# Optimization experiments

Hardware: AMD Instinct MI355X
Metric: run time of the kernel (lower is better)

Reference implementation:

```python
import jax, jax.numpy as jnp
import numpy as np

DIM_IN, DIM_Q, DIM_K, DIM_S, DIM_MLP_S, L, B = 512, 128, 128, 256, 128, 512, 32


def setup_inputs() -> dict:
    key = jax.random.key(0)
    ks = jax.random.split(key, 16)
    s = lambda fan_in: 1.0 / np.sqrt(fan_in)
    inp = {
        "query": jax.random.normal(ks[0], (B, L, DIM_IN), jnp.float32),
        "key": jax.random.normal(ks[1], (B, L, DIM_IN), jnp.float32),
        "value": jax.random.normal(ks[2], (B, L, DIM_IN), jnp.float32),
        "sf": jax.random.normal(ks[3], (B, DIM_S), jnp.float32),
        "atten_mask": jax.random.randint(ks[4], (B, L, L), 0, 2).astype(bool),
        # linear weights stored (in, out); y = x @ W + b
        "Wq": jax.random.normal(ks[5], (DIM_IN, DIM_Q), jnp.float32) * s(DIM_IN),
        "bq": jnp.zeros((DIM_Q,), jnp.float32),
        "Wk": jax.random.normal(ks[6], (DIM_IN, DIM_K), jnp.float32) * s(DIM_IN),
        "bk": jnp.zeros((DIM_K,), jnp.float32),
        "Wv": jax.random.normal(ks[7], (DIM_IN, DIM_K), jnp.float32) * s(DIM_IN),
        "bv": jnp.zeros((DIM_K,), jnp.float32),
        "Wb1": jax.random.normal(ks[8], (DIM_S, DIM_MLP_S), jnp.float32) * s(DIM_S),
        "bb1": jnp.zeros((DIM_MLP_S,), jnp.float32),
        "Wb2": jax.random.normal(ks[9], (DIM_MLP_S, L * L), jnp.float32) * s(DIM_MLP_S),
        "bb2": jnp.zeros((L * L,), jnp.float32),
    }
    return inp


def reference(query, key, value, sf, atten_mask, Wq, bq, Wk, bk, Wv, bv, Wb1, bb1, Wb2, bb2):
    b, l, d = query.shape
    q = query @ Wq + bq          # [b, l, dim_q]
    k = key @ Wk + bk            # [b, l, dim_k]
    v = value @ Wv + bv          # [b, l, dim_k]
    # bias MLP: Linear -> ReLU -> Linear, reshaped to [b, l, l]
    bias = (jax.nn.relu(sf @ Wb1 + bb1) @ Wb2 + bb2).reshape(b, l, l)
    scale = q.shape[-1] ** 0.5
    scores = jnp.einsum("bld,bmd->blm", q, k) / scale
    # faithful to masked_fill_(mask, 1e-9): masked positions become 1e-9, NOT -inf
    scores = jnp.where(atten_mask, jnp.asarray(1e-9, scores.dtype), scores)
    attn = jax.nn.softmax(scores, axis=-1) + bias   # bias added AFTER softmax
    out = jnp.einsum("blm,bmd->bld", attn, v)
    return out
```

## Files before the change

kernel.cpp:

```cpp
#include <hip/hip_runtime.h>


typedef unsigned int   u32;
typedef unsigned short u16;
typedef __attribute__((ext_vector_type(8))) short bf16x8;
typedef __attribute__((ext_vector_type(4))) float f32x4;
typedef __attribute__((ext_vector_type(4))) u32   u32x4;

__device__ __forceinline__ float B2F(u16 x) { return __uint_as_float(((u32)x) << 16); }
__device__ __forceinline__ u16 f2bf(float f) {
    u32 u = __float_as_uint(f);
    return (u16)((u + 0x7fffu + ((u >> 16) & 1u)) >> 16);
}

__global__ __launch_bounds__(256) void prep(
    const void* __restrict__ mask, u32* __restrict__ flag, int detN,
    const float* __restrict__ Wq, const float* __restrict__ Wk, const float* __restrict__ Wv,
    u16* __restrict__ WT,
    const float* __restrict__ sf, const float* __restrict__ Wb1,
    const float* __restrict__ bb1, float* __restrict__ hT)
{
    __shared__ u16 Ts[64][136];
    const int blk = blockIdx.x, tid = threadIdx.x;

    if (blk < detN) {
        const u32* m = (const u32*)mask;
        u32 any = 0;
#pragma unroll
        for (int it = 0; it < 16; ++it) {
            const size_t t = ((size_t)blk * 16 + it) * 256 + tid;
#pragma unroll
            for (int l = 0; l < 4; ++l) any |= (m[t * 4 + l] > 1u) ? 1u : 0u;
        }
        if (__ballot(any)) {
            if ((tid & 63) == 0) atomicOr(flag, 1u);
        }
        return;
    }
    if (blk < detN + 24) {
        const int widx = blk - detN;
        const int s = widx >> 3, kt = widx & 7;
        const float* W = (s == 0) ? Wq : (s == 1) ? Wk : Wv;
        {
            const int kk = tid >> 2, nseg = tid & 3;
            const float4* src = (const float4*)(W + (size_t)(kt * 64 + kk) * 128 + nseg * 32);
#pragma unroll
            for (int j = 0; j < 8; ++j) {
                float4 v = src[j];
                Ts[kk][nseg * 32 + j * 4 + 0] = f2bf(v.x);
                Ts[kk][nseg * 32 + j * 4 + 1] = f2bf(v.y);
                Ts[kk][nseg * 32 + j * 4 + 2] = f2bf(v.z);
                Ts[kk][nseg * 32 + j * 4 + 3] = f2bf(v.w);
            }
        }
        __syncthreads();
        {
            const int n = tid >> 1, kseg = tid & 1;
            u32 pk[16];
#pragma unroll
            for (int j = 0; j < 16; ++j)
                pk[j] = (u32)Ts[kseg * 32 + 2 * j][n] | ((u32)Ts[kseg * 32 + 2 * j + 1][n] << 16);
            u32x4* dst = (u32x4*)(WT + (size_t)s * 65536 + (size_t)n * 512 + kt * 64 + kseg * 32);
            dst[0] = (u32x4){pk[0], pk[1], pk[2], pk[3]};
            dst[1] = (u32x4){pk[4], pk[5], pk[6], pk[7]};
            dst[2] = (u32x4){pk[8], pk[9], pk[10], pk[11]};
            dst[3] = (u32x4){pk[12], pk[13], pk[14], pk[15]};
        }
        return;
    }
    {
        const int t = (blk - detN - 24) * 256 + tid;
        const int b = t >> 7, n = t & 127;
        float acc = bb1[n];
        for (int m = 0; m < 256; ++m)
            acc += sf[b * 256 + m] * Wb1[m * 128 + n];
        hT[n * 32 + b] = fmaxf(acc, 0.0f);
    }
}

__global__ __launch_bounds__(256) void mid(
    const float* __restrict__ Xq, const float* __restrict__ Xk, const float* __restrict__ Xv,
    const u16* __restrict__ WT,
    const float* __restrict__ Bq, const float* __restrict__ Bk, const float* __restrict__ Bv,
    u16* __restrict__ Yq, u16* __restrict__ Yk, u16* __restrict__ YvT,
    const float* __restrict__ hT, const float* __restrict__ Wb2,
    const float* __restrict__ bb2, u16* __restrict__ biasb,
    const void* __restrict__ mask, const u32* __restrict__ flag, int mode,
    int docanon, unsigned char* __restrict__ canonbuf)
{
    __shared__ u16 Xs[64][72];
    const int blk = blockIdx.x, tid = threadIdx.x;

    if (blk < 1024) {
        const size_t n = (size_t)blk * 256 + tid;
        float acc[32];
        {
            const float bb = bb2[n];
#pragma unroll
            for (int b = 0; b < 32; ++b) acc[b] = bb;
        }
#pragma unroll 16
        for (int m = 0; m < 128; ++m) {
            const float wv = Wb2[(size_t)m * 262144 + n];
            const float* hrow = hT + m * 32;
#pragma unroll
            for (int b = 0; b < 32; ++b) acc[b] += wv * hrow[b];
        }
#pragma unroll
        for (int b = 0; b < 32; ++b)
            biasb[(size_t)b * 262144 + n] = f2bf(acc[b]);
        return;
    }

    if (blk < 1792) {
        const int pidx = blk - 1024;
        const int s = pidx >> 8;
        const int R0 = (pidx & 255) * 64;
        const float* X; const float* Bi;
        if (s == 0)      { X = Xq; Bi = Bq; }
        else if (s == 1) { X = Xk; Bi = Bk; }
        else             { X = Xv; Bi = Bv; }
        const u16* Wn = WT + (size_t)s * 65536;

        const int w    = tid >> 6;
        const int lane = tid & 63;
        const int c    = lane & 15;
        const int qd   = lane >> 4;

        f32x4 acc[8];
#pragma unroll
        for (int t = 0; t < 8; ++t) acc[t] = (f32x4){0.f, 0.f, 0.f, 0.f};

        for (int kc = 0; kc < 8; ++kc) {
            __syncthreads();
            {
                const int row = tid >> 2, seg = tid & 3;
                const float4* src = (const float4*)(X + (size_t)(R0 + row) * 512 + kc * 64 + seg * 16);
                float4 v0 = src[0], v1 = src[1], v2 = src[2], v3 = src[3];
                u32 pk[8];
                pk[0] = (u32)f2bf(v0.x) | ((u32)f2bf(v0.y) << 16);
                pk[1] = (u32)f2bf(v0.z) | ((u32)f2bf(v0.w) << 16);
                pk[2] = (u32)f2bf(v1.x) | ((u32)f2bf(v1.y) << 16);
                pk[3] = (u32)f2bf(v1.z) | ((u32)f2bf(v1.w) << 16);
                pk[4] = (u32)f2bf(v2.x) | ((u32)f2bf(v2.y) << 16);
                pk[5] = (u32)f2bf(v2.z) | ((u32)f2bf(v2.w) << 16);
                pk[6] = (u32)f2bf(v3.x) | ((u32)f2bf(v3.y) << 16);
                pk[7] = (u32)f2bf(v3.z) | ((u32)f2bf(v3.w) << 16);
                u32x4* dst = (u32x4*)&Xs[row][seg * 16];
                dst[0] = (u32x4){pk[0], pk[1], pk[2], pk[3]};
                dst[1] = (u32x4){pk[4], pk[5], pk[6], pk[7]};
            }
            __syncthreads();

#pragma unroll
            for (int ks = 0; ks < 2; ++ks) {
                if (s < 2) {
                    const bf16x8 a = *(const bf16x8*)&Xs[w * 16 + c][ks * 32 + qd * 8];
#pragma unroll
                    for (int nt = 0; nt < 8; ++nt) {
                        const bf16x8 b = *(const bf16x8*)(Wn + (size_t)(nt * 16 + c) * 512
                                                          + kc * 64 + ks * 32 + qd * 8);
                        acc[nt] = __builtin_amdgcn_mfma_f32_16x16x32_bf16(a, b, acc[nt], 0, 0, 0);
                    }
                } else {
#pragma unroll
                    for (int t = 0; t < 2; ++t) {
                        const bf16x8 a = *(const bf16x8*)(Wn + (size_t)((2 * w + t) * 16 + c) * 512
                                                          + kc * 64 + ks * 32 + qd * 8);
#pragma unroll
                        for (int it = 0; it < 4; ++it) {
                            const bf16x8 b = *(const bf16x8*)&Xs[it * 16 + c][ks * 32 + qd * 8];
                            acc[t * 4 + it] = __builtin_amdgcn_mfma_f32_16x16x32_bf16(a, b, acc[t * 4 + it], 0, 0, 0);
                        }
                    }
                }
            }
        }

        if (s < 2) {
            u16* Y = (s == 0) ? Yq : Yk;
#pragma unroll
            for (int nt = 0; nt < 8; ++nt) {
                const float bn = Bi[nt * 16 + c];
#pragma unroll
                for (int r = 0; r < 4; ++r)
                    Y[(size_t)(R0 + w * 16 + qd * 4 + r) * 128 + nt * 16 + c] = f2bf(acc[nt][r] + bn);
            }
        } else {
            const int bb = (pidx & 255) >> 3, il0 = R0 & 511;
#pragma unroll
            for (int t = 0; t < 2; ++t)
#pragma unroll
                for (int r = 0; r < 4; ++r) {
                    const int d = (2 * w + t) * 16 + qd * 4 + r;
                    const float bd = Bi[d];
#pragma unroll
                    for (int it = 0; it < 4; ++it)
                        YvT[(size_t)bb * 65536 + (size_t)d * 512 + il0 + it * 16 + c] =
                            f2bf(acc[t * 4 + it][r] + bd);
                }
        }
        return;
    }

    if (docanon) {
        const int cb = blk - 1792;
        const bool i32src = (mode == 2) || (mode == 0 && *flag == 0);
#pragma unroll
        for (int it = 0; it < 8; ++it) {
            const size_t base = ((size_t)cb * 8 + it) * 4096 + (size_t)tid * 16;
            u32 wq[4];
            if (i32src) {
                const int* mi = (const int*)mask + base;
#pragma unroll
                for (int q = 0; q < 4; ++q) {
                    const int4 v = *(const int4*)(mi + q * 4);
                    wq[q] = (v.x ? 1u : 0u) | ((v.y ? 1u : 0u) << 8)
                          | ((v.z ? 1u : 0u) << 16) | ((v.w ? 1u : 0u) << 24);
                }
            } else {
                const u32x4 v = *(const u32x4*)((const unsigned char*)mask + base);
#pragma unroll
                for (int q = 0; q < 4; ++q) {
                    const u32 x = v[q];
                    wq[q] = (((x & 0x7F7F7F7Fu) + 0x7F7F7F7Fu) | x) >> 7 & 0x01010101u;
                }
            }
            *(u32x4*)(canonbuf + base) = (u32x4){wq[0], wq[1], wq[2], wq[3]};
        }
    }
}

__global__ __launch_bounds__(512, 2) void attn_mfma8(
    const u16* __restrict__ qb, const u16* __restrict__ kb, const u16* __restrict__ vTb,
    const unsigned char* __restrict__ canon, const u16* __restrict__ biasb,
    float* __restrict__ out)
{
    __shared__ alignas(16) u16 Ks[2][64 * 136];
    __shared__ alignas(16) u16 Ps[2][64 * 72];
    __shared__ alignas(16) u16 Vs[2][128 * 72];
    __shared__ alignas(16) u16 Bs[2][64 * 72];
    __shared__ float redm[2][64];
    __shared__ float reds[2][64];

    const int tid  = threadIdx.x;
    const int g    = tid >> 8;
    const int gtid = tid & 255;
    const int wl   = (tid >> 6) & 3;
    const int lane = tid & 63;
    const int c    = lane & 15;
    const int qd   = lane >> 4;
    const int bb   = blockIdx.x & 31;
    const int it   = blockIdx.x >> 5;
    const int i0   = it * 64;

    bf16x8 qf[4];
    {
        const u16* qp = qb + ((size_t)bb * 512 + i0 + wl * 16 + c) * 128 + qd * 8;
#pragma unroll
        for (int kc = 0; kc < 4; ++kc) qf[kc] = *(const bf16x8*)(qp + kc * 32);
    }

    const int kr_ = gtid >> 2, ksg = gtid & 3;
    const u16* kbase = kb + ((size_t)bb * 512 + g * 256) * 128;
    {
        const u32x4* src = (const u32x4*)(kbase + (size_t)kr_ * 128 + ksg * 32);
        u32x4 k0 = src[0], k1 = src[1], k2 = src[2], k3 = src[3];
        u32x4* dst = (u32x4*)&Ks[g][kr_ * 136 + ksg * 32];
        dst[0] = k0; dst[1] = k1; dst[2] = k2; dst[3] = k3;
    }
    __syncthreads();

    f32x4 S[4][4];
#pragma unroll
    for (int jt = 0; jt < 4; ++jt)
#pragma unroll
        for (int jj = 0; jj < 4; ++jj) S[jt][jj] = (f32x4){0.f, 0.f, 0.f, 0.f};

#pragma unroll
    for (int jt = 0; jt < 4; ++jt) {
        u32x4 k0, k1, k2, k3;
        if (jt < 3) {
            const u32x4* src = (const u32x4*)(kbase + ((size_t)(jt + 1) * 64 + kr_) * 128 + ksg * 32);
            k0 = src[0]; k1 = src[1]; k2 = src[2]; k3 = src[3];
        }
#pragma unroll
        for (int kc = 0; kc < 4; ++kc) {
            const bf16x8 a = qf[kc];
#pragma unroll
            for (int jj = 0; jj < 4; ++jj) {
                const bf16x8 b = *(const bf16x8*)&Ks[g][(jj * 16 + c) * 136 + kc * 32 + qd * 8];
                S[jt][jj] = __builtin_amdgcn_mfma_f32_16x16x32_bf16(a, b, S[jt][jj], 0, 0, 0);
            }
        }
        if (jt < 3) {
            __syncthreads();
            u32x4* dst = (u32x4*)&Ks[g][kr_ * 136 + ksg * 32];
            dst[0] = k0; dst[1] = k1; dst[2] = k2; dst[3] = k3;
            __syncthreads();
        }
    }

    const int vd = gtid >> 1, vsg = gtid & 1;
    const int brw = gtid >> 2, bsg = gtid & 3;
    const u16* vbase = vTb + (size_t)bb * 65536;
    const u16* bbase = biasb + (size_t)bb * 262144;
    u32x4 vr0, vr1, vr2, vr3, br0, br1;
    {
        const u32x4* sv = (const u32x4*)(vbase + (size_t)vd * 512 + (g * 4) * 64 + vsg * 32);
        vr0 = sv[0]; vr1 = sv[1]; vr2 = sv[2]; vr3 = sv[3];
        const u32x4* sb = (const u32x4*)(bbase + (size_t)(i0 + brw) * 512 + (g * 4) * 64 + bsg * 16);
        br0 = sb[0]; br1 = sb[1];
    }

    const float sc = 0.08838834764831845f;
    float lm[4];
#pragma unroll
    for (int r = 0; r < 4; ++r) {
        const int lrow = wl * 16 + qd * 4 + r;
        const unsigned char* cp = canon + ((size_t)bb * 512 + i0 + lrow) * 512 + g * 256;
        float mx = -3.4e38f;
#pragma unroll
        for (int jt = 0; jt < 4; ++jt)
#pragma unroll
            for (int jj = 0; jj < 4; ++jj) {
                float s = S[jt][jj][r] * sc;
                if (cp[jt * 64 + jj * 16 + c]) s = 1e-9f;
                S[jt][jj][r] = s;
                mx = fmaxf(mx, s);
            }
#pragma unroll
        for (int o = 1; o < 16; o <<= 1) mx = fmaxf(mx, __shfl_xor(mx, o, 64));
        lm[r] = mx;
    }
    if (c == 0) {
#pragma unroll
        for (int r = 0; r < 4; ++r) redm[g][wl * 16 + qd * 4 + r] = lm[r];
    }
    __syncthreads();
    float ls[4];
#pragma unroll
    for (int r = 0; r < 4; ++r) {
        const int lrow = wl * 16 + qd * 4 + r;
        const float gmx = fmaxf(redm[0][lrow], redm[1][lrow]);
        float sm = 0.f;
#pragma unroll
        for (int jt = 0; jt < 4; ++jt)
#pragma unroll
            for (int jj = 0; jj < 4; ++jj) {
                const float e = __expf(S[jt][jj][r] - gmx);
                S[jt][jj][r] = e;
                sm += e;
            }
#pragma unroll
        for (int o = 1; o < 16; o <<= 1) sm += __shfl_xor(sm, o, 64);
        ls[r] = sm;
    }
    if (c == 0) {
#pragma unroll
        for (int r = 0; r < 4; ++r) reds[g][wl * 16 + qd * 4 + r] = ls[r];
    }
    __syncthreads();
    float inv_[4];
#pragma unroll
    for (int r = 0; r < 4; ++r) {
        const int lrow = wl * 16 + qd * 4 + r;
        inv_[r] = 1.0f / (reds[0][lrow] + reds[1][lrow]);
    }

    f32x4 O_[8];
#pragma unroll
    for (int ns = 0; ns < 8; ++ns) O_[ns] = (f32x4){0.f, 0.f, 0.f, 0.f};

#pragma unroll
    for (int jt = 0; jt < 4; ++jt) {
        __syncthreads();
        {
            u32x4* dv = (u32x4*)&Vs[g][vd * 72 + vsg * 32];
            dv[0] = vr0; dv[1] = vr1; dv[2] = vr2; dv[3] = vr3;
            u32x4* db = (u32x4*)&Bs[g][brw * 72 + bsg * 16];
            db[0] = br0; db[1] = br1;
        }
        __syncthreads();
        if (jt < 3) {
            const int tg = g * 4 + jt + 1;
            const u32x4* sv = (const u32x4*)(vbase + (size_t)vd * 512 + tg * 64 + vsg * 32);
            vr0 = sv[0]; vr1 = sv[1]; vr2 = sv[2]; vr3 = sv[3];
            const u32x4* sb = (const u32x4*)(bbase + (size_t)(i0 + brw) * 512 + tg * 64 + bsg * 16);
            br0 = sb[0]; br1 = sb[1];
        }
#pragma unroll
        for (int r = 0; r < 4; ++r) {
            const int lrow = wl * 16 + qd * 4 + r;
#pragma unroll
            for (int jj = 0; jj < 4; ++jj) {
                const float p = S[jt][jj][r] * inv_[r] + B2F(Bs[g][lrow * 72 + jj * 16 + c]);
                Ps[g][lrow * 72 + jj * 16 + c] = f2bf(p);
            }
        }
        __syncthreads();
#pragma unroll
        for (int kc = 0; kc < 2; ++kc) {
            const bf16x8 a = *(const bf16x8*)&Ps[g][(wl * 16 + c) * 72 + kc * 32 + qd * 8];
#pragma unroll
            for (int ns = 0; ns < 8; ++ns) {
                const bf16x8 b = *(const bf16x8*)&Vs[g][(ns * 16 + c) * 72 + kc * 32 + qd * 8];
                O_[ns] = __builtin_amdgcn_mfma_f32_16x16x32_bf16(a, b, O_[ns], 0, 0, 0);
            }
        }
    }

    __syncthreads();
    float* Oc = (float*)&Ks[0][0];
    if (g == 1) {
#pragma unroll
        for (int ns = 0; ns < 8; ++ns)
#pragma unroll
            for (int r = 0; r < 4; ++r)
                Oc[(wl * 16 + qd * 4 + r) * 128 + ns * 16 + c] = O_[ns][r];
    }
    __syncthreads();
    if (g == 0) {
#pragma unroll
        for (int ns = 0; ns < 8; ++ns)
#pragma unroll
            for (int r = 0; r < 4; ++r)
                Oc[(wl * 16 + qd * 4 + r) * 128 + ns * 16 + c] += O_[ns][r];
    }
    __syncthreads();
    {
        const int row = tid >> 3, sg = tid & 7;
        const float4* s4 = (const float4*)&Oc[row * 128 + sg * 16];
        float4* d4 = (float4*)(out + ((size_t)bb * 512 + i0 + row) * 128 + sg * 16);
        d4[0] = s4[0]; d4[1] = s4[1]; d4[2] = s4[2]; d4[3] = s4[3];
    }
}

extern "C" void kernel_launch(void* const* d_in, const int* in_sizes, int n_in,
                              void* d_out, int out_size, void* d_ws, size_t ws_size,
                              hipStream_t stream)
{
    const float* query = (const float*)d_in[0];
    const float* key_  = (const float*)d_in[1];
    const float* value = (const float*)d_in[2];
    const float* sf    = (const float*)d_in[3];
    const void*  mask  = d_in[4];
    const float* Wq  = (const float*)d_in[5];
    const float* bq  = (const float*)d_in[6];
    const float* Wk  = (const float*)d_in[7];
    const float* bk  = (const float*)d_in[8];
    const float* Wv  = (const float*)d_in[9];
    const float* bv  = (const float*)d_in[10];
    const float* Wb1 = (const float*)d_in[11];
    const float* bb1 = (const float*)d_in[12];
    const float* Wb2 = (const float*)d_in[13];
    const float* bb2 = (const float*)d_in[14];
    float* out = (float*)d_out;

    char* w = (char*)d_ws;
    u32*   flag     = (u32*)(w);
    unsigned char* canonbuf = (unsigned char*)(w + (1u << 20));
    u16*   qb    = (u16*)(w + (16u << 20));
    u16*   kb    = (u16*)(w + (24u << 20));
    u16*   vTb   = (u16*)(w + (32u << 20));
    float* hT    = (float*)(w + (40u << 20));
    u16*   biasb = (u16*)(w + (41u << 20));
    u16*   WT    = (u16*)(w + (58u << 20));

    int mode = 0;
    if (n_in >= 15 && in_sizes[0] == 33554432) {
        if (in_sizes[4] == 8388608)       mode = 1;
        else if (in_sizes[4] == 33554432) mode = 2;
    }
    if (mode == 0) hipMemsetAsync(flag, 0, 4, stream);

    const int detN = (mode == 0) ? 128 : 0;
    prep<<<detN + 40, 256, 0, stream>>>(mask, flag, detN, Wq, Wk, Wv, WT,
                                        sf, Wb1, bb1, hT);

    const int docanon = (mode != 1) ? 1 : 0;
    mid<<<2048, 256, 0, stream>>>(query, key_, value, WT,
                                  bq, bk, bv, qb, kb, vTb,
                                  hT, Wb2, bb2, biasb,
                                  mask, flag, mode, docanon, canonbuf);

    const unsigned char* canon = (mode == 1) ? (const unsigned char*)mask : canonbuf;
    attn_mfma8<<<256, 512, 0, stream>>>(qb, kb, vTb, canon, biasb, out);
}
```

Measured before the change: 358.1 us.

## Split attention into 32-row blocks with four key groups; stage projection weights in LDS

The attention kernel now processes 32 query rows per block, split across four 128-key groups instead of two 256-key groups. Grid size doubles to 512 blocks and launch bounds allow four blocks per SM. K and V^T are read straight from global memory rather than staged through LDS, which removes several barriers and the software prefetch. The projection kernel also stages each weight tile in LDS instead of reading it repeatedly from global memory, at the cost of more LDS use and a four-way output reduction.

New measurement: 368.0 us. 2.8% more time.

```diff
diff --git a/kernel.cpp b/kernel.cpp
--- a/kernel.cpp
+++ b/kernel.cpp
@@ -89,6 +89,7 @@
     int docanon, unsigned char* __restrict__ canonbuf)
 {
     __shared__ u16 Xs[64][72];
+    __shared__ u16 Ws[128][72];
     const int blk = blockIdx.x, tid = threadIdx.x;
 
     if (blk < 1024) {
@@ -150,6 +151,13 @@
                 dst[0] = (u32x4){pk[0], pk[1], pk[2], pk[3]};
                 dst[1] = (u32x4){pk[4], pk[5], pk[6], pk[7]};
             }
+            {
+                const int n = tid >> 1, seg = tid & 1;
+                const u32x4* src = (const u32x4*)(Wn + (size_t)n * 512 + kc * 64 + seg * 32);
+                u32x4 v0 = src[0], v1 = src[1], v2 = src[2], v3 = src[3];
+                u32x4* dst = (u32x4*)&Ws[n][seg * 32];
+                dst[0] = v0; dst[1] = v1; dst[2] = v2; dst[3] = v3;
+            }
             __syncthreads();
 
 #pragma unroll
@@ -158,15 +166,13 @@
                     const bf16x8 a = *(const bf16x8*)&Xs[w * 16 + c][ks * 32 + qd * 8];
 #pragma unroll
                     for (int nt = 0; nt < 8; ++nt) {
-                        const bf16x8 b = *(const bf16x8*)(Wn + (size_t)(nt * 16 + c) * 512
-                                                          + kc * 64 + ks * 32 + qd * 8);
+                        const bf16x8 b = *(const bf16x8*)&Ws[nt * 16 + c][ks * 32 + qd * 8];
                         acc[nt] = __builtin_amdgcn_mfma_f32_16x16x32_bf16(a, b, acc[nt], 0, 0, 0);
                     }
                 } else {
 #pragma unroll
                     for (int t = 0; t < 2; ++t) {
-                        const bf16x8 a = *(const bf16x8*)(Wn + (size_t)((2 * w + t) * 16 + c) * 512
-                                                          + kc * 64 + ks * 32 + qd * 8);
+                        const bf16x8 a = *(const bf16x8*)&Ws[(2 * w + t) * 16 + c][ks * 32 + qd * 8];
 #pragma unroll
                         for (int it = 0; it < 4; ++it) {
                             const bf16x8 b = *(const bf16x8*)&Xs[it * 16 + c][ks * 32 + qd * 8];
@@ -231,28 +237,26 @@
     }
 }
 
-__global__ __launch_bounds__(512, 2) void attn_mfma8(
+__global__ __launch_bounds__(512, 4) void attn4(
     const u16* __restrict__ qb, const u16* __restrict__ kb, const u16* __restrict__ vTb,
     const unsigned char* __restrict__ canon, const u16* __restrict__ biasb,
     float* __restrict__ out)
 {
-    __shared__ alignas(16) u16 Ks[2][64 * 136];
-    __shared__ alignas(16) u16 Ps[2][64 * 72];
-    __shared__ alignas(16) u16 Vs[2][128 * 72];
-    __shared__ alignas(16) u16 Bs[2][64 * 72];
-    __shared__ float redm[2][64];
-    __shared__ float reds[2][64];
+    __shared__ alignas(16) u16 Ps[4][32 * 136];
+    __shared__ alignas(16) u16 Bs[4][32 * 136];
+    __shared__ float redm[4][32];
+    __shared__ float reds[4][32];
 
     const int tid  = threadIdx.x;
-    const int g    = tid >> 8;
-    const int gtid = tid & 255;
-    const int wl   = (tid >> 6) & 3;
+    const int g    = tid >> 7;
+    const int gt   = tid & 127;
+    const int wl   = (tid >> 6) & 1;
     const int lane = tid & 63;
     const int c    = lane & 15;
     const int qd   = lane >> 4;
     const int bb   = blockIdx.x & 31;
     const int it   = blockIdx.x >> 5;
-    const int i0   = it * 64;
+    const int i0   = it * 32;
 
     bf16x8 qf[4];
     {
@@ -261,56 +265,35 @@
         for (int kc = 0; kc < 4; ++kc) qf[kc] = *(const bf16x8*)(qp + kc * 32);
     }
 
-    const int kr_ = gtid >> 2, ksg = gtid & 3;
-    const u16* kbase = kb + ((size_t)bb * 512 + g * 256) * 128;
-    {
-        const u32x4* src = (const u32x4*)(kbase + (size_t)kr_ * 128 + ksg * 32);
-        u32x4 k0 = src[0], k1 = src[1], k2 = src[2], k3 = src[3];
-        u32x4* dst = (u32x4*)&Ks[g][kr_ * 136 + ksg * 32];
-        dst[0] = k0; dst[1] = k1; dst[2] = k2; dst[3] = k3;
-    }
-    __syncthreads();
-
-    f32x4 S[4][4];
-#pragma unroll
-    for (int jt = 0; jt < 4; ++jt)
+    f32x4 S[2][4];
+#pragma unroll
+    for (int jt = 0; jt < 2; ++jt)
 #pragma unroll
         for (int jj = 0; jj < 4; ++jj) S[jt][jj] = (f32x4){0.f, 0.f, 0.f, 0.f};
 
-#pragma unroll
-    for (int jt = 0; jt < 4; ++jt) {
-        u32x4 k0, k1, k2, k3;
-        if (jt < 3) {
-            const u32x4* src = (const u32x4*)(kbase + ((size_t)(jt + 1) * 64 + kr_) * 128 + ksg * 32);
-            k0 = src[0]; k1 = src[1]; k2 = src[2]; k3 = src[3];
-        }
+    const u16* kgb = kb + ((size_t)bb * 512 + g * 128) * 128;
+#pragma unroll
+    for (int jt = 0; jt < 2; ++jt)
 #pragma unroll
         for (int kc = 0; kc < 4; ++kc) {
             const bf16x8 a = qf[kc];
 #pragma unroll
             for (int jj = 0; jj < 4; ++jj) {
-                const bf16x8 b = *(const bf16x8*)&Ks[g][(jj * 16 + c) * 136 + kc * 32 + qd * 8];
+                const bf16x8 b = *(const bf16x8*)(kgb + (size_t)(jt * 64 + jj * 16 + c) * 128
+                                                  + kc * 32 + qd * 8);
                 S[jt][jj] = __builtin_amdgcn_mfma_f32_16x16x32_bf16(a, b, S[jt][jj], 0, 0, 0);
             }
         }
-        if (jt < 3) {
-            __syncthreads();
-            u32x4* dst = (u32x4*)&Ks[g][kr_ * 136 + ksg * 32];
-            dst[0] = k0; dst[1] = k1; dst[2] = k2; dst[3] = k3;
-            __syncthreads();
-        }
-    }
-
-    const int vd = gtid >> 1, vsg = gtid & 1;
-    const int brw = gtid >> 2, bsg = gtid & 3;
-    const u16* vbase = vTb + (size_t)bb * 65536;
-    const u16* bbase = biasb + (size_t)bb * 262144;
-    u32x4 vr0, vr1, vr2, vr3, br0, br1;
+
+    const int brow = gt >> 2, bseg = gt & 3;
+    u32x4 bq0, bq1, bq2, bq3;
     {
-        const u32x4* sv = (const u32x4*)(vbase + (size_t)vd * 512 + (g * 4) * 64 + vsg * 32);
-        vr0 = sv[0]; vr1 = sv[1]; vr2 = sv[2]; vr3 = sv[3];
-        const u32x4* sb = (const u32x4*)(bbase + (size_t)(i0 + brw) * 512 + (g * 4) * 64 + bsg * 16);
-        br0 = sb[0]; br1 = sb[1];
+        const u32x4* sb = (const u32x4*)(biasb + (size_t)bb * 262144
+                          + (size_t)(i0 + brow) * 512 + g * 128 + bseg * 32);
+        bq0 = sb[0]; bq1 = sb[1];
+        const u32x4* sb2 = (const u32x4*)(biasb + (size_t)bb * 262144
+                           + (size_t)(i0 + brow) * 512 + g * 128 + bseg * 32 + 16);
+        bq2 = sb2[0]; bq3 = sb2[1];
     }
 
     const float sc = 0.08838834764831845f;
@@ -318,10 +301,10 @@
 #pragma unroll
     for (int r = 0; r < 4; ++r) {
         const int lrow = wl * 16 + qd * 4 + r;
-        const unsigned char* cp = canon + ((size_t)bb * 512 + i0 + lrow) * 512 + g * 256;
+        const unsigned char* cp = canon + ((size_t)bb * 512 + i0 + lrow) * 512 + g * 128;
         float mx = -3.4e38f;
 #pragma unroll
-        for (int jt = 0; jt < 4; ++jt)
+        for (int jt = 0; jt < 2; ++jt)
 #pragma unroll
             for (int jj = 0; jj < 4; ++jj) {
                 float s = S[jt][jj][r] * sc;
@@ -342,10 +325,11 @@
 #pragma unroll
     for (int r = 0; r < 4; ++r) {
         const int lrow = wl * 16 + qd * 4 + r;
-        const float gmx = fmaxf(redm[0][lrow], redm[1][lrow]);
+        const float gmx = fmaxf(fmaxf(redm[0][lrow], redm[1][lrow]),
+                                fmaxf(redm[2][lrow], redm[3][lrow]));
         float sm = 0.f;
 #pragma unroll
-        for (int jt = 0; jt < 4; ++jt)
+        for (int jt = 0; jt < 2; ++jt)
 #pragma unroll
             for (int jj = 0; jj < 4; ++jj) {
                 const float e = __expf(S[jt][jj][r] - gmx);
@@ -365,54 +349,47 @@
 #pragma unroll
     for (int r = 0; r < 4; ++r) {
         const int lrow = wl * 16 + qd * 4 + r;
-        inv_[r] = 1.0f / (reds[0][lrow] + reds[1][lrow]);
-    }
+        inv_[r] = 1.0f / (reds[0][lrow] + reds[1][lrow] + reds[2][lrow] + reds[3][lrow]);
+    }
+
+    {
+        u32x4* db = (u32x4*)&Bs[g][brow * 136 + bseg * 32];
+        db[0] = bq0; db[1] = bq1; db[2] = bq2; db[3] = bq3;
+    }
+    __syncthreads();
+#pragma unroll
+    for (int r = 0; r < 4; ++r) {
+        const int lrow = wl * 16 + qd * 4 + r;
+#pragma unroll
+        for (int jt = 0; jt < 2; ++jt)
+#pragma unroll
+            for (int jj = 0; jj < 4; ++jj) {
+                const float p = S[jt][jj][r] * inv_[r]
+                              + B2F(Bs[g][lrow * 136 + jt * 64 + jj * 16 + c]);
+                Ps[g][lrow * 136 + jt * 64 + jj * 16 + c] = f2bf(p);
+            }
+    }
+    __syncthreads();
 
     f32x4 O_[8];
 #pragma unroll
     for (int ns = 0; ns < 8; ++ns) O_[ns] = (f32x4){0.f, 0.f, 0.f, 0.f};
 
-#pragma unroll
-    for (int jt = 0; jt < 4; ++jt) {
-        __syncthreads();
-        {
-            u32x4* dv = (u32x4*)&Vs[g][vd * 72 + vsg * 32];
-            dv[0] = vr0; dv[1] = vr1; dv[2] = vr2; dv[3] = vr3;
-            u32x4* db = (u32x4*)&Bs[g][brw * 72 + bsg * 16];
-            db[0] = br0; db[1] = br1;
-        }
-        __syncthreads();
-        if (jt < 3) {
-            const int tg = g * 4 + jt + 1;
-            const u32x4* sv = (const u32x4*)(vbase + (size_t)vd * 512 + tg * 64 + vsg * 32);
-            vr0 = sv[0]; vr1 = sv[1]; vr2 = sv[2]; vr3 = sv[3];
-            const u32x4* sb = (const u32x4*)(bbase + (size_t)(i0 + brw) * 512 + tg * 64 + bsg * 16);
-            br0 = sb[0]; br1 = sb[1];
-        }
-#pragma unroll
-        for (int r = 0; r < 4; ++r) {
-            const int lrow = wl * 16 + qd * 4 + r;
-#pragma unroll
-            for (int jj = 0; jj < 4; ++jj) {
-                const float p = S[jt][jj][r] * inv_[r] + B2F(Bs[g][lrow * 72 + jj * 16 + c]);
-                Ps[g][lrow * 72 + jj * 16 + c] = f2bf(p);
-            }
-        }
-        __syncthreads();
-#pragma unroll
-        for (int kc = 0; kc < 2; ++kc) {
-            const bf16x8 a = *(const bf16x8*)&Ps[g][(wl * 16 + c) * 72 + kc * 32 + qd * 8];
-#pragma unroll
-            for (int ns = 0; ns < 8; ++ns) {
-                const bf16x8 b = *(const bf16x8*)&Vs[g][(ns * 16 + c) * 72 + kc * 32 + qd * 8];
-                O_[ns] = __builtin_amdgcn_mfma_f32_16x16x32_bf16(a, b, O_[ns], 0, 0, 0);
-            }
-        }
-    }
-
-    __syncthreads();
-    float* Oc = (float*)&Ks[0][0];
-    if (g == 1) {
+    const u16* vgb = vTb + (size_t)bb * 65536 + g * 128;
+#pragma unroll
+    for (int kc = 0; kc < 4; ++kc) {
+        const bf16x8 a = *(const bf16x8*)&Ps[g][(wl * 16 + c) * 136 + kc * 32 + qd * 8];
+#pragma unroll
+        for (int ns = 0; ns < 8; ++ns) {
+            const bf16x8 b = *(const bf16x8*)(vgb + (size_t)(ns * 16 + c) * 512
+                                              + kc * 32 + qd * 8);
+            O_[ns] = __builtin_amdgcn_mfma_f32_16x16x32_bf16(a, b, O_[ns], 0, 0, 0);
+        }
+    }
+
+    __syncthreads();
+    float* Oc = (float*)&Ps[0][0];
+    if (g == 3) {
 #pragma unroll
         for (int ns = 0; ns < 8; ++ns)
 #pragma unroll
@@ -420,7 +397,7 @@
                 Oc[(wl * 16 + qd * 4 + r) * 128 + ns * 16 + c] = O_[ns][r];
     }
     __syncthreads();
-    if (g == 0) {
+    if (g == 2) {
 #pragma unroll
         for (int ns = 0; ns < 8; ++ns)
 #pragma unroll
@@ -428,11 +405,27 @@
                 Oc[(wl * 16 + qd * 4 + r) * 128 + ns * 16 + c] += O_[ns][r];
     }
     __syncthreads();
+    if (g == 1) {
+#pragma unroll
+        for (int ns = 0; ns < 8; ++ns)
+#pragma unroll
+            for (int r = 0; r < 4; ++r)
+                Oc[(wl * 16 + qd * 4 + r) * 128 + ns * 16 + c] += O_[ns][r];
+    }
+    __syncthreads();
+    if (g == 0) {
+#pragma unroll
+        for (int ns = 0; ns < 8; ++ns)
+#pragma unroll
+            for (int r = 0; r < 4; ++r)
+                Oc[(wl * 16 + qd * 4 + r) * 128 + ns * 16 + c] += O_[ns][r];
+    }
+    __syncthreads();
     {
-        const int row = tid >> 3, sg = tid & 7;
-        const float4* s4 = (const float4*)&Oc[row * 128 + sg * 16];
-        float4* d4 = (float4*)(out + ((size_t)bb * 512 + i0 + row) * 128 + sg * 16);
-        d4[0] = s4[0]; d4[1] = s4[1]; d4[2] = s4[2]; d4[3] = s4[3];
+        const int row = tid >> 4, sg = tid & 15;
+        const float4* s4 = (const float4*)&Oc[row * 128 + sg * 8];
+        float4* d4 = (float4*)(out + ((size_t)bb * 512 + i0 + row) * 128 + sg * 8);
+        d4[0] = s4[0]; d4[1] = s4[1];
     }
 }
 
@@ -485,5 +478,5 @@
                                   mask, flag, mode, docanon, canonbuf);
 
     const unsigned char* canon = (mode == 1) ? (const unsigned char*)mask : canonbuf;
-    attn_mfma8<<<256, 512, 0, stream>>>(qb, kb, vTb, canon, biasb, out);
+    attn4<<<512, 512, 0, stream>>>(qb, kb, vTb, canon, biasb, out);
 }
```
